# Kernel tuning notes

Hardware: AMD Instinct MI355X
Metric: run time of the kernel (lower is better)

The kernel has to match this reference:

```python
import jax, jax.numpy as jnp
import numpy as np

N_NODES = 100000
N_EDGES = 1600000
F_IN = 64
CONVS = [128, 128, 64]
DECODER_HID = 128
N_CLASSES = 2


def _glorot(key, shape):
    fan_in = shape[1]
    lim = 1.0 / np.sqrt(fan_in)
    return jax.random.uniform(key, shape, jnp.float32, -lim, lim)


def setup_inputs() -> dict:
    key = jax.random.key(0)
    ks = jax.random.split(key, 16)
    x = jax.random.normal(ks[0], (N_NODES, F_IN), jnp.float32)
    edge_index = jax.random.randint(ks[1], (2, N_EDGES), 0, N_NODES, jnp.int32)
    dims = [F_IN] + CONVS  # [64,128,128,64]
    inp = {"x": x, "edge_index": edge_index}
    ki = 2
    for i in range(len(CONVS)):
        d_in, d_out = dims[i], dims[i + 1]
        inp[f"Wl{i}"] = _glorot(ks[ki], (d_out, d_in)); ki += 1
        inp[f"bl{i}"] = jnp.zeros((d_out,), jnp.float32)
        inp[f"Wr{i}"] = _glorot(ks[ki], (d_out, d_in)); ki += 1
    inp["Wd1"] = _glorot(ks[ki], (DECODER_HID, CONVS[-1])); ki += 1
    inp["bd1"] = jnp.zeros((DECODER_HID,), jnp.float32)
    inp["Wd2"] = _glorot(ks[ki], (N_CLASSES, DECODER_HID)); ki += 1
    inp["bd2"] = jnp.zeros((N_CLASSES,), jnp.float32)
    return inp


def _sage_conv(x, src, dst, inv_deg, Wl, bl, Wr):
    # gather source features per edge, scatter-mean onto destinations
    msg = x[src]                                          # [E, F]
    agg = jax.ops.segment_sum(msg, dst, num_segments=N_NODES)
    agg = agg * inv_deg[:, None]                          # mean aggregation
    # out = lin_l(mean_neighbors) + lin_r(x_self)
    return agg @ Wl.T + bl + x @ Wr.T


def reference(x, edge_index, Wl0, bl0, Wr0, Wl1, bl1, Wr1, Wl2, bl2, Wr2, Wd1, bd1, Wd2, bd2):
    src = edge_index[0]
    dst = edge_index[1]
    deg = jax.ops.segment_sum(jnp.ones((src.shape[0],), x.dtype), dst, num_segments=N_NODES)
    inv_deg = jnp.where(deg > 0, 1.0 / jnp.maximum(deg, 1.0), 0.0)
    params = [(Wl0, bl0, Wr0), (Wl1, bl1, Wr1), (Wl2, bl2, Wr2)]
    h = x
    for i, (Wl, bl, Wr) in enumerate(params):
        h = _sage_conv(h, src, dst, inv_deg, Wl, bl, Wr)
        if i != len(params) - 1:
            h = jax.nn.relu(h)
    # decoder: ReLU -> Linear(64,128) -> ReLU -> Linear(128,2)
    h = jax.nn.relu(h)
    h = jax.nn.relu(h @ Wd1.T + bd1)
    return h @ Wd2.T + bd2
```

## Files before the change

### kernel.cpp

```cpp
#include <hip/hip_runtime.h>
#include <cstdint>
#include <cstddef>

#define NN 100000
#define NE 1600000
#define BSH 9
#define NBUCK 196
#define P3_CHUNK 8192
#define P3_BLOCKS 196

typedef __attribute__((ext_vector_type(8))) short short8;
typedef __attribute__((ext_vector_type(4))) float f32x4;


__device__ inline unsigned pack_split(float v) {
    unsigned u = __builtin_bit_cast(unsigned, v);
    unsigned hi = (u + 0x7fffu + ((u >> 16) & 1u)) >> 16;
    float vh = __builtin_bit_cast(float, hi << 16);
    float r = v - vh;
    unsigned u2 = __builtin_bit_cast(unsigned, r);
    unsigned lo = (u2 + 0x7fffu + ((u2 >> 16) & 1u)) >> 16;
    return hi | (lo << 16);
}

__device__ inline float rec_sum(unsigned u) {
    return __builtin_bit_cast(float, u << 16) + __builtin_bit_cast(float, u & 0xffff0000u);
}

__device__ inline void frag_extract(const unsigned* p, short8& hi, short8& lo) {
    uint4 p0 = *(const uint4*)p;
    uint4 p1 = *(const uint4*)(p + 4);
    unsigned h0 = __builtin_amdgcn_perm(p0.y, p0.x, 0x05040100u);
    unsigned l0 = __builtin_amdgcn_perm(p0.y, p0.x, 0x07060302u);
    unsigned h1 = __builtin_amdgcn_perm(p0.w, p0.z, 0x05040100u);
    unsigned l1 = __builtin_amdgcn_perm(p0.w, p0.z, 0x07060302u);
    unsigned h2 = __builtin_amdgcn_perm(p1.y, p1.x, 0x05040100u);
    unsigned l2 = __builtin_amdgcn_perm(p1.y, p1.x, 0x07060302u);
    unsigned h3 = __builtin_amdgcn_perm(p1.w, p1.z, 0x05040100u);
    unsigned l3 = __builtin_amdgcn_perm(p1.w, p1.z, 0x07060302u);
    uint4 H = {h0, h1, h2, h3};
    uint4 L = {l0, l1, l2, l3};
    hi = __builtin_bit_cast(short8, H);
    lo = __builtin_bit_cast(short8, L);
}


__global__ __launch_bounds__(256) void k_zero_small(int* p, int n) {
    for (int i = threadIdx.x; i < n; i += 256) p[i] = 0;
}

__global__ __launch_bounds__(256) void k_hist(const int* __restrict__ dst, int* __restrict__ bcnt) {
    __shared__ int h[NBUCK];
    const int tid = threadIdx.x;
    if (tid < NBUCK) h[tid] = 0;
    __syncthreads();
    for (int e = blockIdx.x * 256 + tid; e < NE; e += gridDim.x * 256)
        atomicAdd(&h[dst[e] >> BSH], 1);
    __syncthreads();
    if (tid < NBUCK) atomicAdd(&bcnt[tid], h[tid]);
}

__global__ __launch_bounds__(256) void k_bscan(const int* __restrict__ bcnt, int* __restrict__ bstart,
                                               int* __restrict__ gcur) {
    __shared__ int sh[256];
    const int t = threadIdx.x;
    int v = (t < NBUCK) ? bcnt[t] : 0;
    sh[t] = v;
    __syncthreads();
    for (int off = 1; off < 256; off <<= 1) {
        int u = 0;
        if (t >= off) u = sh[t - off];
        __syncthreads();
        sh[t] += u;
        __syncthreads();
    }
    int excl = sh[t] - v;
    if (t < NBUCK) { bstart[t] = excl; gcur[t] = excl; }
    if (t == 0) bstart[NBUCK] = NE;
}

__global__ __launch_bounds__(256) void k_partition(const int* __restrict__ srce, const int* __restrict__ dste,
                                                   int* __restrict__ gcur, int* __restrict__ tmp) {
    __shared__ int h[NBUCK], lstart[NBUCK], gbase[NBUCK], scn[256];
    __shared__ int s_pack[P3_CHUNK];
    __shared__ int s_gad[P3_CHUNK];
    const int tid = threadIdx.x;
    const int base = blockIdx.x * P3_CHUNK;
    if (tid < NBUCK) h[tid] = 0;
    __syncthreads();
    int rank[P3_CHUNK / 256];
#pragma unroll
    for (int i = 0; i < P3_CHUNK / 256; i++) {
        int idx = base + i * 256 + tid;
        if (idx < NE) rank[i] = atomicAdd(&h[dste[idx] >> BSH], 1);
    }
    __syncthreads();
    int hv = (tid < NBUCK) ? h[tid] : 0;
    if (tid < NBUCK) gbase[tid] = atomicAdd(&gcur[tid], hv);
    scn[tid] = hv;
    __syncthreads();
    for (int off = 1; off < 256; off <<= 1) {
        int u = 0;
        if (tid >= off) u = scn[tid - off];
        __syncthreads();
        scn[tid] += u;
        __syncthreads();
    }
    if (tid < NBUCK) lstart[tid] = scn[tid] - hv;
    __syncthreads();
#pragma unroll
    for (int i = 0; i < P3_CHUNK / 256; i++) {
        int idx = base + i * 256 + tid;
        if (idx < NE) {
            int d = dste[idx], s = srce[idx];
            int b = d >> BSH;
            int slot = lstart[b] + rank[i];
            s_pack[slot] = (s << BSH) | (d & ((1 << BSH) - 1));
            s_gad[slot] = gbase[b] + rank[i];
        }
    }
    __syncthreads();
    int chunkN = NE - base;
    if (chunkN > P3_CHUNK) chunkN = P3_CHUNK;
#pragma unroll
    for (int i = 0; i < P3_CHUNK / 256; i++) {
        int slot = i * 256 + tid;
        if (slot < chunkN) tmp[s_gad[slot]] = s_pack[slot];
    }
}

__global__ __launch_bounds__(256) void k_bucket(const int* __restrict__ tmp, const int* __restrict__ bstart,
                                                int* __restrict__ row_ptr, int* __restrict__ col,
                                                float* __restrict__ invd) {
    __shared__ int cnt[512], cur[512], scn[256];
    const int b = blockIdx.x, tid = threadIdx.x;
    const int base = bstart[b];
    const int n = bstart[b + 1] - base;
    cnt[tid] = 0;
    cnt[tid + 256] = 0;
    __syncthreads();
    for (int k = tid; k < n; k += 256) atomicAdd(&cnt[tmp[base + k] & 511], 1);
    __syncthreads();
    int c0 = cnt[2 * tid], c1 = cnt[2 * tid + 1], s = c0 + c1;
    scn[tid] = s;
    __syncthreads();
    for (int off = 1; off < 256; off <<= 1) {
        int u = 0;
        if (tid >= off) u = scn[tid - off];
        __syncthreads();
        scn[tid] += u;
        __syncthreads();
    }
    int excl = scn[tid] - s;
    int node = (b << BSH) + 2 * tid;
    if (node < NN) {
        row_ptr[node] = base + excl;
        invd[node] = c0 ? 1.0f / (float)c0 : 0.0f;
    }
    if (node + 1 < NN) {
        row_ptr[node + 1] = base + excl + c0;
        invd[node + 1] = c1 ? 1.0f / (float)c1 : 0.0f;
    }
    cur[2 * tid] = base + excl;
    cur[2 * tid + 1] = base + excl + c0;
    if (b == 0 && tid == 0) row_ptr[NN] = NE;
    __syncthreads();
    for (int k = tid; k < n; k += 256) {
        int p = tmp[base + k];
        int pos = atomicAdd(&cur[p & 511], 1);
        col[pos] = p >> BSH;
    }
}


__global__ __launch_bounds__(256) void k_xsplit(const float* __restrict__ x, unsigned* __restrict__ Xp) {
    int i = blockIdx.x * 256 + threadIdx.x;
    float4 v = ((const float4*)x)[i];
    uint4 o = {pack_split(v.x), pack_split(v.y), pack_split(v.z), pack_split(v.w)};
    ((uint4*)Xp)[i] = o;
}

__global__ __launch_bounds__(256) void k_wsplit(const float* __restrict__ Wl0, const float* __restrict__ Wr0,
                                                const float* __restrict__ Wl1, const float* __restrict__ Wr1,
                                                const float* __restrict__ Wl2, const float* __restrict__ Wr2,
                                                const float* __restrict__ Wd1, const float* __restrict__ bl2,
                                                unsigned* __restrict__ Wp, float* __restrict__ biasPQ) {
    int i = blockIdx.x * 256 + threadIdx.x;
    if (i < 8192) Wp[i] = pack_split(Wl0[i]);
    else if (i < 16384) Wp[i] = pack_split(Wr0[i - 8192]);
    else if (i < 32768) Wp[i] = pack_split(Wl1[i - 16384]);
    else if (i < 49152) Wp[i] = pack_split(Wr1[i - 32768]);
    else if (i < 57344) Wp[i] = pack_split(Wl2[i - 49152]);
    else if (i < 65536) Wp[i] = pack_split(Wr2[i - 57344]);
    else if (i < 73728) Wp[i] = pack_split(Wd1[i - 65536]);
    else if (i < 73856) {
        int j = i - 73728;
        biasPQ[j] = (j < 64) ? 0.f : bl2[j - 64];
    }
}


__global__ __launch_bounds__(256) void k_agg64(const float* __restrict__ h, const int* __restrict__ row_ptr,
                                               const int* __restrict__ col, const float* __restrict__ inv_deg,
                                               unsigned* __restrict__ agg) {
    int node = blockIdx.x * 4 + (threadIdx.x >> 6);
    int lane = threadIdx.x & 63;
    int start = row_ptr[node], end = row_ptr[node + 1];
    float a0 = 0.f, a1 = 0.f, a2 = 0.f, a3 = 0.f, a4 = 0.f, a5 = 0.f, a6 = 0.f, a7 = 0.f;
    for (int cs = start; cs < end; cs += 64) {
        int n = end - cs;
        if (n > 64) n = 64;
        int my = (lane < n) ? col[cs + lane] : 0;
        int j = 0;
        for (; j + 8 <= n; j += 8) {
            int s0 = __shfl(my, j + 0), s1 = __shfl(my, j + 1);
            int s2 = __shfl(my, j + 2), s3 = __shfl(my, j + 3);
            int s4 = __shfl(my, j + 4), s5 = __shfl(my, j + 5);
            int s6 = __shfl(my, j + 6), s7 = __shfl(my, j + 7);
            float v0 = h[(size_t)s0 * 64 + lane];
            float v1 = h[(size_t)s1 * 64 + lane];
            float v2 = h[(size_t)s2 * 64 + lane];
            float v3 = h[(size_t)s3 * 64 + lane];
            float v4 = h[(size_t)s4 * 64 + lane];
            float v5 = h[(size_t)s5 * 64 + lane];
            float v6 = h[(size_t)s6 * 64 + lane];
            float v7 = h[(size_t)s7 * 64 + lane];
            a0 += v0; a1 += v1; a2 += v2; a3 += v3;
            a4 += v4; a5 += v5; a6 += v6; a7 += v7;
        }
        for (; j < n; j++) {
            int s = __shfl(my, j);
            a0 += h[(size_t)s * 64 + lane];
        }
    }
    float acc = ((a0 + a1) + (a2 + a3)) + ((a4 + a5) + (a6 + a7));
    agg[(size_t)node * 64 + lane] = pack_split(acc * inv_deg[node]);
}

__global__ __launch_bounds__(256) void k_agg128p(const unsigned* __restrict__ hp, const int* __restrict__ row_ptr,
                                                 const int* __restrict__ col, const float* __restrict__ inv_deg,
                                                 unsigned* __restrict__ agg) {
    int node = blockIdx.x * 4 + (threadIdx.x >> 6);
    int lane = threadIdx.x & 63;
    int start = row_ptr[node], end = row_ptr[node + 1];
    const uint2* h2 = (const uint2*)hp;
    float ax0 = 0.f, ax1 = 0.f, ax2 = 0.f, ax3 = 0.f, ax4 = 0.f, ax5 = 0.f, ax6 = 0.f, ax7 = 0.f;
    float ay0 = 0.f, ay1 = 0.f, ay2 = 0.f, ay3 = 0.f, ay4 = 0.f, ay5 = 0.f, ay6 = 0.f, ay7 = 0.f;
    for (int cs = start; cs < end; cs += 64) {
        int n = end - cs;
        if (n > 64) n = 64;
        int my = (lane < n) ? col[cs + lane] : 0;
        int j = 0;
        for (; j + 8 <= n; j += 8) {
            int s0 = __shfl(my, j + 0), s1 = __shfl(my, j + 1);
            int s2 = __shfl(my, j + 2), s3 = __shfl(my, j + 3);
            int s4 = __shfl(my, j + 4), s5 = __shfl(my, j + 5);
            int s6 = __shfl(my, j + 6), s7 = __shfl(my, j + 7);
            uint2 u0 = h2[(size_t)s0 * 64 + lane];
            uint2 u1 = h2[(size_t)s1 * 64 + lane];
            uint2 u2 = h2[(size_t)s2 * 64 + lane];
            uint2 u3 = h2[(size_t)s3 * 64 + lane];
            uint2 u4 = h2[(size_t)s4 * 64 + lane];
            uint2 u5 = h2[(size_t)s5 * 64 + lane];
            uint2 u6 = h2[(size_t)s6 * 64 + lane];
            uint2 u7 = h2[(size_t)s7 * 64 + lane];
            ax0 += rec_sum(u0.x); ay0 += rec_sum(u0.y);
            ax1 += rec_sum(u1.x); ay1 += rec_sum(u1.y);
            ax2 += rec_sum(u2.x); ay2 += rec_sum(u2.y);
            ax3 += rec_sum(u3.x); ay3 += rec_sum(u3.y);
            ax4 += rec_sum(u4.x); ay4 += rec_sum(u4.y);
            ax5 += rec_sum(u5.x); ay5 += rec_sum(u5.y);
            ax6 += rec_sum(u6.x); ay6 += rec_sum(u6.y);
            ax7 += rec_sum(u7.x); ay7 += rec_sum(u7.y);
        }
        for (; j < n; j++) {
            int s = __shfl(my, j);
            uint2 u = h2[(size_t)s * 64 + lane];
            ax0 += rec_sum(u.x);
            ay0 += rec_sum(u.y);
        }
    }
    float w = inv_deg[node];
    float sx = (((ax0 + ax1) + (ax2 + ax3)) + ((ax4 + ax5) + (ax6 + ax7))) * w;
    float sy = (((ay0 + ay1) + (ay2 + ay3)) + ((ay4 + ay5) + (ay6 + ay7))) * w;
    uint2 o = {pack_split(sx), pack_split(sy)};
    *((uint2*)agg + (size_t)node * 64 + lane) = o;
}

__global__ __launch_bounds__(256) void k_agg_relu64p(const float* __restrict__ PQ, const int* __restrict__ row_ptr,
                                                     const int* __restrict__ col, const float* __restrict__ inv_deg,
                                                     unsigned* __restrict__ out) {
    int node = blockIdx.x * 4 + (threadIdx.x >> 6);
    int lane = threadIdx.x & 63;
    int start = row_ptr[node], end = row_ptr[node + 1];
    float a0 = 0.f, a1 = 0.f, a2 = 0.f, a3 = 0.f, a4 = 0.f, a5 = 0.f, a6 = 0.f, a7 = 0.f;
    for (int cs = start; cs < end; cs += 64) {
        int n = end - cs;
        if (n > 64) n = 64;
        int my = (lane < n) ? col[cs + lane] : 0;
        int j = 0;
        for (; j + 8 <= n; j += 8) {
            int s0 = __shfl(my, j + 0), s1 = __shfl(my, j + 1);
            int s2 = __shfl(my, j + 2), s3 = __shfl(my, j + 3);
            int s4 = __shfl(my, j + 4), s5 = __shfl(my, j + 5);
            int s6 = __shfl(my, j + 6), s7 = __shfl(my, j + 7);
            float v0 = PQ[(size_t)s0 * 128 + lane];
            float v1 = PQ[(size_t)s1 * 128 + lane];
            float v2 = PQ[(size_t)s2 * 128 + lane];
            float v3 = PQ[(size_t)s3 * 128 + lane];
            float v4 = PQ[(size_t)s4 * 128 + lane];
            float v5 = PQ[(size_t)s5 * 128 + lane];
            float v6 = PQ[(size_t)s6 * 128 + lane];
            float v7 = PQ[(size_t)s7 * 128 + lane];
            a0 += v0; a1 += v1; a2 += v2; a3 += v3;
            a4 += v4; a5 += v5; a6 += v6; a7 += v7;
        }
        for (; j < n; j++) {
            int s = __shfl(my, j);
            a0 += PQ[(size_t)s * 128 + lane];
        }
    }
    float acc = ((a0 + a1) + (a2 + a3)) + ((a4 + a5) + (a6 + a7));
    float v = PQ[(size_t)node * 128 + 64 + lane] + inv_deg[node] * acc;
    out[(size_t)node * 64 + lane] = pack_split(fmaxf(v, 0.f));
}


#define LDL 36

template <int K>
__device__ inline void mg_phase(const unsigned* __restrict__ A, const unsigned* __restrict__ W,
                                int m0, unsigned* Al, unsigned* Bl, f32x4 (&acc)[4][4],
                                int tid, int wm, int wn, int l15, int quad) {
    const int srow = tid >> 1, scol = (tid & 1) * 16;
#pragma unroll 1
    for (int kt = 0; kt < K; kt += 32) {
        __syncthreads();
        uint4 a0 = {0, 0, 0, 0}, a1 = {0, 0, 0, 0}, a2 = {0, 0, 0, 0}, a3 = {0, 0, 0, 0};
        int gr = m0 + srow;
        if (gr < NN) {
            const uint4* p = (const uint4*)(A + (size_t)gr * K + kt + scol);
            a0 = p[0]; a1 = p[1]; a2 = p[2]; a3 = p[3];
        }
        const uint4* q = (const uint4*)(W + srow * K + kt + scol);
        uint4 b0 = q[0], b1 = q[1], b2 = q[2], b3 = q[3];
        uint4* da = (uint4*)(Al + srow * LDL + scol);
        da[0] = a0; da[1] = a1; da[2] = a2; da[3] = a3;
        uint4* db = (uint4*)(Bl + srow * LDL + scol);
        db[0] = b0; db[1] = b1; db[2] = b2; db[3] = b3;
        __syncthreads();
        short8 ah[4], al[4], bh[4], bl[4];
#pragma unroll
        for (int t = 0; t < 4; t++) {
            frag_extract(Al + (wm + t * 16 + l15) * LDL + quad * 8, ah[t], al[t]);
            frag_extract(Bl + (wn + t * 16 + l15) * LDL + quad * 8, bh[t], bl[t]);
        }
#pragma unroll
        for (int mt = 0; mt < 4; mt++)
#pragma unroll
            for (int nt = 0; nt < 4; nt++) {
                acc[mt][nt] = __builtin_amdgcn_mfma_f32_16x16x32_bf16(ah[mt], bh[nt], acc[mt][nt], 0, 0, 0);
                acc[mt][nt] = __builtin_amdgcn_mfma_f32_16x16x32_bf16(ah[mt], bl[nt], acc[mt][nt], 0, 0, 0);
                acc[mt][nt] = __builtin_amdgcn_mfma_f32_16x16x32_bf16(al[mt], bh[nt], acc[mt][nt], 0, 0, 0);
            }
    }
}

template <int K1, int K2, bool RELU, int OMODE>
__global__ __launch_bounds__(256) void k_mgemm(const unsigned* __restrict__ A1, const unsigned* __restrict__ W1,
                                               const unsigned* A2, const unsigned* __restrict__ W2,
                                               const float* __restrict__ bias, float* Cf, unsigned* Cp) {
    __shared__ unsigned Al[128 * LDL];
    __shared__ unsigned Bl[128 * LDL];
    const int tid = threadIdx.x;
    const int m0 = blockIdx.x * 128;
    const int wave = tid >> 6, lane = tid & 63;
    const int wm = (wave & 1) * 64, wn = (wave >> 1) * 64;
    const int l15 = lane & 15, quad = lane >> 4;
    f32x4 acc[4][4];
#pragma unroll
    for (int i = 0; i < 4; i++)
#pragma unroll
        for (int j = 0; j < 4; j++) acc[i][j] = (f32x4){0.f, 0.f, 0.f, 0.f};

    mg_phase<K1>(A1, W1, m0, Al, Bl, acc, tid, wm, wn, l15, quad);
    if (K2 > 0) mg_phase<K2>(A2, W2, m0, Al, Bl, acc, tid, wm, wn, l15, quad);

#pragma unroll
    for (int mt = 0; mt < 4; mt++) {
        int rbase = m0 + wm + mt * 16 + quad * 4;
#pragma unroll
        for (int nt = 0; nt < 4; nt++) {
            int cg = wn + nt * 16 + l15;
            float bv = bias[cg];
#pragma unroll
            for (int r = 0; r < 4; r++) {
                int row = rbase + r;
                if (row < NN) {
                    float v = acc[mt][nt][r] + bv;
                    if (RELU) v = fmaxf(v, 0.f);
                    if (OMODE == 0) Cf[(size_t)row * 128 + cg] = v;
                    else Cp[(size_t)row * 128 + cg] = pack_split(v);
                }
            }
        }
    }
}


__global__ __launch_bounds__(256) void k_dec2(const float* __restrict__ h, const float* __restrict__ W,
                                              const float* __restrict__ b, float* __restrict__ out) {
    int node = blockIdx.x * 4 + (threadIdx.x >> 6);
    int lane = threadIdx.x & 63;
    float2 hv = *((const float2*)(h + (size_t)node * 128) + lane);
    float d0 = hv.x * W[2 * lane] + hv.y * W[2 * lane + 1];
    float d1 = hv.x * W[128 + 2 * lane] + hv.y * W[128 + 2 * lane + 1];
    for (int off = 32; off > 0; off >>= 1) {
        d0 += __shfl_down(d0, off);
        d1 += __shfl_down(d1, off);
    }
    if (lane == 0) {
        out[(size_t)node * 2 + 0] = d0 + b[0];
        out[(size_t)node * 2 + 1] = d1 + b[1];
    }
}


extern "C" void kernel_launch(void* const* d_in, const int* in_sizes, int n_in,
                              void* d_out, int out_size, void* d_ws, size_t ws_size,
                              hipStream_t stream) {
    const float* x   = (const float*)d_in[0];
    const int*   ei  = (const int*)d_in[1];
    const float* Wl0 = (const float*)d_in[2];
    const float* bl0 = (const float*)d_in[3];
    const float* Wr0 = (const float*)d_in[4];
    const float* Wl1 = (const float*)d_in[5];
    const float* bl1 = (const float*)d_in[6];
    const float* Wr1 = (const float*)d_in[7];
    const float* Wl2 = (const float*)d_in[8];
    const float* bl2 = (const float*)d_in[9];
    const float* Wr2 = (const float*)d_in[10];
    const float* Wd1 = (const float*)d_in[11];
    const float* bd1 = (const float*)d_in[12];
    const float* Wd2 = (const float*)d_in[13];
    const float* bd2 = (const float*)d_in[14];
    float* out = (float*)d_out;

    char* ws = (char*)d_ws;
    size_t off = 0;
    auto alloc = [&](size_t bytes) {
        char* p = ws + off;
        off = (off + bytes + 255) & ~(size_t)255;
        return p;
    };
    int*      bcnt    = (int*)alloc((size_t)NBUCK * 4);
    int*      bstart  = (int*)alloc((size_t)(NBUCK + 1) * 4);
    int*      gcur    = (int*)alloc((size_t)NBUCK * 4);
    int*      row_ptr = (int*)alloc((size_t)(NN + 1) * 4);
    float*    invd    = (float*)alloc((size_t)NN * 4);
    int*      col     = (int*)alloc((size_t)NE * 4);
    unsigned* Wp      = (unsigned*)alloc((size_t)73728 * 4);
    float*    biasPQ  = (float*)alloc(128 * 4);
    unsigned* S1      = (unsigned*)alloc((size_t)NN * 128 * 4);
    unsigned* S2      = (unsigned*)alloc((size_t)NN * 128 * 4);
    (void)ws_size;

    int*      tmp   = (int*)S2;
    unsigned* Xp    = S1;
    unsigned* Agg0p = S1 + (size_t)NN * 64;
    unsigned* G0p   = S2;
    unsigned* Agg1p = S1;
    unsigned* H1p   = S2;
    float*    PQ    = (float*)S1;
    unsigned* h2p   = S2;
    float*    d1    = (float*)S1;

    const unsigned* WL0p = Wp;
    const unsigned* WR0p = Wp + 8192;
    const unsigned* WL1p = Wp + 16384;
    const unsigned* WR1p = Wp + 32768;
    const unsigned* WPQp = Wp + 49152;
    const unsigned* WD1p = Wp + 65536;

    const int* srce = ei;
    const int* dste = ei + NE;

    k_zero_small<<<1, 256, 0, stream>>>(bcnt, NBUCK);
    k_hist<<<400, 256, 0, stream>>>(dste, bcnt);
    k_bscan<<<1, 256, 0, stream>>>(bcnt, bstart, gcur);
    k_partition<<<P3_BLOCKS, 256, 0, stream>>>(srce, dste, gcur, tmp);
    k_bucket<<<NBUCK, 256, 0, stream>>>(tmp, bstart, row_ptr, col, invd);

    k_wsplit<<<289, 256, 0, stream>>>(Wl0, Wr0, Wl1, Wr1, Wl2, Wr2, Wd1, bl2, Wp, biasPQ);
    k_xsplit<<<(NN * 64 / 4 + 255) / 256, 256, 0, stream>>>(x, Xp);

    const int gGemm = (NN + 127) / 128;
    const int gNode = NN / 4;

    k_agg64<<<gNode, 256, 0, stream>>>(x, row_ptr, col, invd, Agg0p);
    k_mgemm<64, 64, true, 1><<<gGemm, 256, 0, stream>>>(Agg0p, WL0p, Xp, WR0p, bl0, nullptr, G0p);

    k_agg128p<<<gNode, 256, 0, stream>>>(G0p, row_ptr, col, invd, Agg1p);
    k_mgemm<128, 128, true, 1><<<gGemm, 256, 0, stream>>>(Agg1p, WL1p, G0p, WR1p, bl1, nullptr, H1p);

    k_mgemm<128, 0, false, 0><<<gGemm, 256, 0, stream>>>(H1p, WPQp, nullptr, nullptr, biasPQ, PQ, nullptr);
    k_agg_relu64p<<<gNode, 256, 0, stream>>>(PQ, row_ptr, col, invd, h2p);

    k_mgemm<64, 0, true, 0><<<gGemm, 256, 0, stream>>>(h2p, WD1p, nullptr, nullptr, bd1, d1, nullptr);
    k_dec2<<<gNode, 256, 0, stream>>>(d1, Wd2, bd2, out);
}
```

Before: 548.3 us.

## Gather bf16-high features in aggregations and store hi/lo planes separately

```diff
diff --git a/kernel.cpp b/kernel.cpp
--- a/kernel.cpp
+++ b/kernel.cpp
@@ -23,25 +23,13 @@
     return hi | (lo << 16);
 }
 
-__device__ inline float rec_sum(unsigned u) {
-    return __builtin_bit_cast(float, u << 16) + __builtin_bit_cast(float, u & 0xffff0000u);
-}
-
-__device__ inline void frag_extract(const unsigned* p, short8& hi, short8& lo) {
-    uint4 p0 = *(const uint4*)p;
-    uint4 p1 = *(const uint4*)(p + 4);
-    unsigned h0 = __builtin_amdgcn_perm(p0.y, p0.x, 0x05040100u);
-    unsigned l0 = __builtin_amdgcn_perm(p0.y, p0.x, 0x07060302u);
-    unsigned h1 = __builtin_amdgcn_perm(p0.w, p0.z, 0x05040100u);
-    unsigned l1 = __builtin_amdgcn_perm(p0.w, p0.z, 0x07060302u);
-    unsigned h2 = __builtin_amdgcn_perm(p1.y, p1.x, 0x05040100u);
-    unsigned l2 = __builtin_amdgcn_perm(p1.y, p1.x, 0x07060302u);
-    unsigned h3 = __builtin_amdgcn_perm(p1.w, p1.z, 0x05040100u);
-    unsigned l3 = __builtin_amdgcn_perm(p1.w, p1.z, 0x07060302u);
-    uint4 H = {h0, h1, h2, h3};
-    uint4 L = {l0, l1, l2, l3};
-    hi = __builtin_bit_cast(short8, H);
-    lo = __builtin_bit_cast(short8, L);
+__device__ inline unsigned short rnb(float v) {
+    unsigned u = __builtin_bit_cast(unsigned, v);
+    return (unsigned short)((u + 0x7fffu + ((u >> 16) & 1u)) >> 16);
+}
+
+__device__ inline float bf2f(unsigned short u) {
+    return __builtin_bit_cast(float, (unsigned)u << 16);
 }
 
 
@@ -173,36 +161,45 @@
 }
 
 
-__global__ __launch_bounds__(256) void k_xsplit(const float* __restrict__ x, unsigned* __restrict__ Xp) {
+__global__ __launch_bounds__(256) void k_xhi(const float* __restrict__ x, unsigned short* __restrict__ Xh) {
     int i = blockIdx.x * 256 + threadIdx.x;
     float4 v = ((const float4*)x)[i];
-    uint4 o = {pack_split(v.x), pack_split(v.y), pack_split(v.z), pack_split(v.w)};
-    ((uint4*)Xp)[i] = o;
+    ushort4 o = {rnb(v.x), rnb(v.y), rnb(v.z), rnb(v.w)};
+    ((ushort4*)Xh)[i] = o;
 }
 
 __global__ __launch_bounds__(256) void k_wsplit(const float* __restrict__ Wl0, const float* __restrict__ Wr0,
                                                 const float* __restrict__ Wl1, const float* __restrict__ Wr1,
                                                 const float* __restrict__ Wl2, const float* __restrict__ Wr2,
                                                 const float* __restrict__ Wd1, const float* __restrict__ bl2,
-                                                unsigned* __restrict__ Wp, float* __restrict__ biasPQ) {
+                                                unsigned short* __restrict__ Wh, unsigned short* __restrict__ Wl,
+                                                float* __restrict__ biasPQ) {
     int i = blockIdx.x * 256 + threadIdx.x;
-    if (i < 8192) Wp[i] = pack_split(Wl0[i]);
-    else if (i < 16384) Wp[i] = pack_split(Wr0[i - 8192]);
-    else if (i < 32768) Wp[i] = pack_split(Wl1[i - 16384]);
-    else if (i < 49152) Wp[i] = pack_split(Wr1[i - 32768]);
-    else if (i < 57344) Wp[i] = pack_split(Wl2[i - 49152]);
-    else if (i < 65536) Wp[i] = pack_split(Wr2[i - 57344]);
-    else if (i < 73728) Wp[i] = pack_split(Wd1[i - 65536]);
-    else if (i < 73856) {
+    float v = 0.f;
+    bool valid = true;
+    if (i < 8192) v = Wl0[i];
+    else if (i < 16384) v = Wr0[i - 8192];
+    else if (i < 32768) v = Wl1[i - 16384];
+    else if (i < 49152) v = Wr1[i - 32768];
+    else if (i < 57344) v = Wl2[i - 49152];
+    else if (i < 65536) v = Wr2[i - 57344];
+    else if (i < 73728) v = Wd1[i - 65536];
+    else valid = false;
+    if (valid) {
+        unsigned ps = pack_split(v);
+        Wh[i] = (unsigned short)ps;
+        Wl[i] = (unsigned short)(ps >> 16);
+    }
+    if (i >= 73728 && i < 73856) {
         int j = i - 73728;
         biasPQ[j] = (j < 64) ? 0.f : bl2[j - 64];
     }
 }
 
 
-__global__ __launch_bounds__(256) void k_agg64(const float* __restrict__ h, const int* __restrict__ row_ptr,
-                                               const int* __restrict__ col, const float* __restrict__ inv_deg,
-                                               unsigned* __restrict__ agg) {
+__global__ __launch_bounds__(256) void k_agg64h(const unsigned short* __restrict__ Xh, const int* __restrict__ row_ptr,
+                                                const int* __restrict__ col, const float* __restrict__ invd,
+                                                unsigned short* __restrict__ Ah, unsigned short* __restrict__ Al) {
     int node = blockIdx.x * 4 + (threadIdx.x >> 6);
     int lane = threadIdx.x & 63;
     int start = row_ptr[node], end = row_ptr[node + 1];
@@ -217,33 +214,34 @@
             int s2 = __shfl(my, j + 2), s3 = __shfl(my, j + 3);
             int s4 = __shfl(my, j + 4), s5 = __shfl(my, j + 5);
             int s6 = __shfl(my, j + 6), s7 = __shfl(my, j + 7);
-            float v0 = h[(size_t)s0 * 64 + lane];
-            float v1 = h[(size_t)s1 * 64 + lane];
-            float v2 = h[(size_t)s2 * 64 + lane];
-            float v3 = h[(size_t)s3 * 64 + lane];
-            float v4 = h[(size_t)s4 * 64 + lane];
-            float v5 = h[(size_t)s5 * 64 + lane];
-            float v6 = h[(size_t)s6 * 64 + lane];
-            float v7 = h[(size_t)s7 * 64 + lane];
+            float v0 = bf2f(Xh[(size_t)s0 * 64 + lane]);
+            float v1 = bf2f(Xh[(size_t)s1 * 64 + lane]);
+            float v2 = bf2f(Xh[(size_t)s2 * 64 + lane]);
+            float v3 = bf2f(Xh[(size_t)s3 * 64 + lane]);
+            float v4 = bf2f(Xh[(size_t)s4 * 64 + lane]);
+            float v5 = bf2f(Xh[(size_t)s5 * 64 + lane]);
+            float v6 = bf2f(Xh[(size_t)s6 * 64 + lane]);
+            float v7 = bf2f(Xh[(size_t)s7 * 64 + lane]);
             a0 += v0; a1 += v1; a2 += v2; a3 += v3;
             a4 += v4; a5 += v5; a6 += v6; a7 += v7;
         }
         for (; j < n; j++) {
             int s = __shfl(my, j);
-            a0 += h[(size_t)s * 64 + lane];
+            a0 += bf2f(Xh[(size_t)s * 64 + lane]);
         }
     }
     float acc = ((a0 + a1) + (a2 + a3)) + ((a4 + a5) + (a6 + a7));
-    agg[(size_t)node * 64 + lane] = pack_split(acc * inv_deg[node]);
-}
-
-__global__ __launch_bounds__(256) void k_agg128p(const unsigned* __restrict__ hp, const int* __restrict__ row_ptr,
-                                                 const int* __restrict__ col, const float* __restrict__ inv_deg,
-                                                 unsigned* __restrict__ agg) {
+    unsigned ps = pack_split(acc * invd[node]);
+    Ah[(size_t)node * 64 + lane] = (unsigned short)ps;
+    Al[(size_t)node * 64 + lane] = (unsigned short)(ps >> 16);
+}
+
+__global__ __launch_bounds__(256) void k_agg128h(const unsigned short* __restrict__ Gh, const int* __restrict__ row_ptr,
+                                                 const int* __restrict__ col, const float* __restrict__ invd,
+                                                 unsigned short* __restrict__ Ah, unsigned short* __restrict__ Al) {
     int node = blockIdx.x * 4 + (threadIdx.x >> 6);
     int lane = threadIdx.x & 63;
     int start = row_ptr[node], end = row_ptr[node + 1];
-    const uint2* h2 = (const uint2*)hp;
     float ax0 = 0.f, ax1 = 0.f, ax2 = 0.f, ax3 = 0.f, ax4 = 0.f, ax5 = 0.f, ax6 = 0.f, ax7 = 0.f;
     float ay0 = 0.f, ay1 = 0.f, ay2 = 0.f, ay3 = 0.f, ay4 = 0.f, ay5 = 0.f, ay6 = 0.f, ay7 = 0.f;
     for (int cs = start; cs < end; cs += 64) {
@@ -256,40 +254,42 @@
             int s2 = __shfl(my, j + 2), s3 = __shfl(my, j + 3);
             int s4 = __shfl(my, j + 4), s5 = __shfl(my, j + 5);
             int s6 = __shfl(my, j + 6), s7 = __shfl(my, j + 7);
-            uint2 u0 = h2[(size_t)s0 * 64 + lane];
-            uint2 u1 = h2[(size_t)s1 * 64 + lane];
-            uint2 u2 = h2[(size_t)s2 * 64 + lane];
-            uint2 u3 = h2[(size_t)s3 * 64 + lane];
-            uint2 u4 = h2[(size_t)s4 * 64 + lane];
-            uint2 u5 = h2[(size_t)s5 * 64 + lane];
-            uint2 u6 = h2[(size_t)s6 * 64 + lane];
-            uint2 u7 = h2[(size_t)s7 * 64 + lane];
-            ax0 += rec_sum(u0.x); ay0 += rec_sum(u0.y);
-            ax1 += rec_sum(u1.x); ay1 += rec_sum(u1.y);
-            ax2 += rec_sum(u2.x); ay2 += rec_sum(u2.y);
-            ax3 += rec_sum(u3.x); ay3 += rec_sum(u3.y);
-            ax4 += rec_sum(u4.x); ay4 += rec_sum(u4.y);
-            ax5 += rec_sum(u5.x); ay5 += rec_sum(u5.y);
-            ax6 += rec_sum(u6.x); ay6 += rec_sum(u6.y);
-            ax7 += rec_sum(u7.x); ay7 += rec_sum(u7.y);
+            unsigned u0 = *(const unsigned*)(Gh + (size_t)s0 * 128 + 2 * lane);
+            unsigned u1 = *(const unsigned*)(Gh + (size_t)s1 * 128 + 2 * lane);
+            unsigned u2 = *(const unsigned*)(Gh + (size_t)s2 * 128 + 2 * lane);
+            unsigned u3 = *(const unsigned*)(Gh + (size_t)s3 * 128 + 2 * lane);
+            unsigned u4 = *(const unsigned*)(Gh + (size_t)s4 * 128 + 2 * lane);
+            unsigned u5 = *(const unsigned*)(Gh + (size_t)s5 * 128 + 2 * lane);
+            unsigned u6 = *(const unsigned*)(Gh + (size_t)s6 * 128 + 2 * lane);
+            unsigned u7 = *(const unsigned*)(Gh + (size_t)s7 * 128 + 2 * lane);
+            ax0 += bf2f((unsigned short)u0); ay0 += bf2f((unsigned short)(u0 >> 16));
+            ax1 += bf2f((unsigned short)u1); ay1 += bf2f((unsigned short)(u1 >> 16));
+            ax2 += bf2f((unsigned short)u2); ay2 += bf2f((unsigned short)(u2 >> 16));
+            ax3 += bf2f((unsigned short)u3); ay3 += bf2f((unsigned short)(u3 >> 16));
+            ax4 += bf2f((unsigned short)u4); ay4 += bf2f((unsigned short)(u4 >> 16));
+            ax5 += bf2f((unsigned short)u5); ay5 += bf2f((unsigned short)(u5 >> 16));
+            ax6 += bf2f((unsigned short)u6); ay6 += bf2f((unsigned short)(u6 >> 16));
+            ax7 += bf2f((unsigned short)u7); ay7 += bf2f((unsigned short)(u7 >> 16));
         }
         for (; j < n; j++) {
             int s = __shfl(my, j);
-            uint2 u = h2[(size_t)s * 64 + lane];
-            ax0 += rec_sum(u.x);
-            ay0 += rec_sum(u.y);
-        }
-    }
-    float w = inv_deg[node];
+            unsigned u = *(const unsigned*)(Gh + (size_t)s * 128 + 2 * lane);
+            ax0 += bf2f((unsigned short)u);
+            ay0 += bf2f((unsigned short)(u >> 16));
+        }
+    }
+    float w = invd[node];
     float sx = (((ax0 + ax1) + (ax2 + ax3)) + ((ax4 + ax5) + (ax6 + ax7))) * w;
     float sy = (((ay0 + ay1) + (ay2 + ay3)) + ((ay4 + ay5) + (ay6 + ay7))) * w;
-    uint2 o = {pack_split(sx), pack_split(sy)};
-    *((uint2*)agg + (size_t)node * 64 + lane) = o;
-}
-
-__global__ __launch_bounds__(256) void k_agg_relu64p(const float* __restrict__ PQ, const int* __restrict__ row_ptr,
-                                                     const int* __restrict__ col, const float* __restrict__ inv_deg,
-                                                     unsigned* __restrict__ out) {
+    unsigned px = pack_split(sx), py = pack_split(sy);
+    *(unsigned*)(Ah + (size_t)node * 128 + 2 * lane) = (px & 0xffffu) | (py << 16);
+    *(unsigned*)(Al + (size_t)node * 128 + 2 * lane) = (px >> 16) | (py & 0xffff0000u);
+}
+
+__global__ __launch_bounds__(256) void k_aggPh(const unsigned short* __restrict__ Ph, const float* __restrict__ Qf,
+                                               const int* __restrict__ row_ptr, const int* __restrict__ col,
+                                               const float* __restrict__ invd,
+                                               unsigned short* __restrict__ Hh, unsigned short* __restrict__ Hl) {
     int node = blockIdx.x * 4 + (threadIdx.x >> 6);
     int lane = threadIdx.x & 63;
     int start = row_ptr[node], end = row_ptr[node + 1];
@@ -304,56 +304,85 @@
             int s2 = __shfl(my, j + 2), s3 = __shfl(my, j + 3);
             int s4 = __shfl(my, j + 4), s5 = __shfl(my, j + 5);
             int s6 = __shfl(my, j + 6), s7 = __shfl(my, j + 7);
-            float v0 = PQ[(size_t)s0 * 128 + lane];
-            float v1 = PQ[(size_t)s1 * 128 + lane];
-            float v2 = PQ[(size_t)s2 * 128 + lane];
-            float v3 = PQ[(size_t)s3 * 128 + lane];
-            float v4 = PQ[(size_t)s4 * 128 + lane];
-            float v5 = PQ[(size_t)s5 * 128 + lane];
-            float v6 = PQ[(size_t)s6 * 128 + lane];
-            float v7 = PQ[(size_t)s7 * 128 + lane];
+            float v0 = bf2f(Ph[(size_t)s0 * 64 + lane]);
+            float v1 = bf2f(Ph[(size_t)s1 * 64 + lane]);
+            float v2 = bf2f(Ph[(size_t)s2 * 64 + lane]);
+            float v3 = bf2f(Ph[(size_t)s3 * 64 + lane]);
+            float v4 = bf2f(Ph[(size_t)s4 * 64 + lane]);
+            float v5 = bf2f(Ph[(size_t)s5 * 64 + lane]);
+            float v6 = bf2f(Ph[(size_t)s6 * 64 + lane]);
+            float v7 = bf2f(Ph[(size_t)s7 * 64 + lane]);
             a0 += v0; a1 += v1; a2 += v2; a3 += v3;
             a4 += v4; a5 += v5; a6 += v6; a7 += v7;
         }
         for (; j < n; j++) {
             int s = __shfl(my, j);
-            a0 += PQ[(size_t)s * 128 + lane];
+            a0 += bf2f(Ph[(size_t)s * 64 + lane]);
         }
     }
     float acc = ((a0 + a1) + (a2 + a3)) + ((a4 + a5) + (a6 + a7));
-    float v = PQ[(size_t)node * 128 + 64 + lane] + inv_deg[node] * acc;
-    out[(size_t)node * 64 + lane] = pack_split(fmaxf(v, 0.f));
-}
-
-
-#define LDL 36
-
-template <int K>
-__device__ inline void mg_phase(const unsigned* __restrict__ A, const unsigned* __restrict__ W,
-                                int m0, unsigned* Al, unsigned* Bl, f32x4 (&acc)[4][4],
-                                int tid, int wm, int wn, int l15, int quad) {
-    const int srow = tid >> 1, scol = (tid & 1) * 16;
+    float v = Qf[(size_t)node * 64 + lane] + invd[node] * acc;
+    unsigned ps = pack_split(fmaxf(v, 0.f));
+    Hh[(size_t)node * 64 + lane] = (unsigned short)ps;
+    Hl[(size_t)node * 64 + lane] = (unsigned short)(ps >> 16);
+}
+
+
+#define LA 40
+
+template <int K, int AFMT>
+__device__ inline void mgp(const unsigned short* __restrict__ Ah_g, const unsigned short* __restrict__ Al_g,
+                           const float* __restrict__ Af_g,
+                           const unsigned short* __restrict__ Wh_g, const unsigned short* __restrict__ Wl_g,
+                           int m0, unsigned short* sAh, unsigned short* sAl,
+                           unsigned short* sBh, unsigned short* sBl,
+                           f32x4 (&acc)[4][4], int tid, int wm, int wn, int l15, int quad) {
+    const int srow = tid >> 1, sc = (tid & 1) * 16;
 #pragma unroll 1
     for (int kt = 0; kt < K; kt += 32) {
         __syncthreads();
-        uint4 a0 = {0, 0, 0, 0}, a1 = {0, 0, 0, 0}, a2 = {0, 0, 0, 0}, a3 = {0, 0, 0, 0};
         int gr = m0 + srow;
-        if (gr < NN) {
-            const uint4* p = (const uint4*)(A + (size_t)gr * K + kt + scol);
-            a0 = p[0]; a1 = p[1]; a2 = p[2]; a3 = p[3];
-        }
-        const uint4* q = (const uint4*)(W + srow * K + kt + scol);
-        uint4 b0 = q[0], b1 = q[1], b2 = q[2], b3 = q[3];
-        uint4* da = (uint4*)(Al + srow * LDL + scol);
-        da[0] = a0; da[1] = a1; da[2] = a2; da[3] = a3;
-        uint4* db = (uint4*)(Bl + srow * LDL + scol);
-        db[0] = b0; db[1] = b1; db[2] = b2; db[3] = b3;
+        uint4 h0 = {0, 0, 0, 0}, h1 = {0, 0, 0, 0}, l0 = {0, 0, 0, 0}, l1 = {0, 0, 0, 0};
+        if (AFMT == 0) {
+            if (gr < NN) {
+                const uint4* ph = (const uint4*)(Ah_g + (size_t)gr * K + kt + sc);
+                h0 = ph[0]; h1 = ph[1];
+                const uint4* pl = (const uint4*)(Al_g + (size_t)gr * K + kt + sc);
+                l0 = pl[0]; l1 = pl[1];
+            }
+        } else {
+            if (gr < NN) {
+                const float4* pf = (const float4*)(Af_g + (size_t)gr * K + kt + sc);
+                float4 f0 = pf[0], f1 = pf[1], f2 = pf[2], f3 = pf[3];
+                float fs[16] = {f0.x, f0.y, f0.z, f0.w, f1.x, f1.y, f1.z, f1.w,
+                                f2.x, f2.y, f2.z, f2.w, f3.x, f3.y, f3.z, f3.w};
+                alignas(16) unsigned short hh[16], ll[16];
+#pragma unroll
+                for (int i = 0; i < 16; i++) {
+                    unsigned ps = pack_split(fs[i]);
+                    hh[i] = (unsigned short)ps;
+                    ll[i] = (unsigned short)(ps >> 16);
+                }
+                h0 = *(const uint4*)&hh[0]; h1 = *(const uint4*)&hh[8];
+                l0 = *(const uint4*)&ll[0]; l1 = *(const uint4*)&ll[8];
+            }
+        }
+        const uint4* qh = (const uint4*)(Wh_g + srow * K + kt + sc);
+        uint4 b0 = qh[0], b1 = qh[1];
+        const uint4* ql = (const uint4*)(Wl_g + srow * K + kt + sc);
+        uint4 b2 = ql[0], b3 = ql[1];
+        *(uint4*)(sAh + srow * LA + sc) = h0; *(uint4*)(sAh + srow * LA + sc + 8) = h1;
+        *(uint4*)(sAl + srow * LA + sc) = l0; *(uint4*)(sAl + srow * LA + sc + 8) = l1;
+        *(uint4*)(sBh + srow * LA + sc) = b0; *(uint4*)(sBh + srow * LA + sc + 8) = b1;
+        *(uint4*)(sBl + srow * LA + sc) = b2; *(uint4*)(sBl + srow * LA + sc + 8) = b3;
         __syncthreads();
         short8 ah[4], al[4], bh[4], bl[4];
 #pragma unroll
         for (int t = 0; t < 4; t++) {
-            frag_extract(Al + (wm + t * 16 + l15) * LDL + quad * 8, ah[t], al[t]);
-            frag_extract(Bl + (wn + t * 16 + l15) * LDL + quad * 8, bh[t], bl[t]);
+            ah[t] = *(const short8*)(sAh + (wm + t * 16 + l15) * LA + quad * 8);
+            al[t] = *(const short8*)(sAl + (wm + t * 16 + l15) * LA + quad * 8);
+            bh[t] = *(const short8*)(sBh + (wn + t * 16 + l15) * LA + quad * 8);
+            bl[t] = *(const short8*)(sBl + (wn + t * 16 + l15) * LA + quad * 8);
         }
 #pragma unroll
         for (int mt = 0; mt < 4; mt++)
@@ -366,12 +395,15 @@
     }
 }
 
-template <int K1, int K2, bool RELU, int OMODE>
-__global__ __launch_bounds__(256) void k_mgemm(const unsigned* __restrict__ A1, const unsigned* __restrict__ W1,
-                                               const unsigned* A2, const unsigned* __restrict__ W2,
-                                               const float* __restrict__ bias, float* Cf, unsigned* Cp) {
-    __shared__ unsigned Al[128 * LDL];
-    __shared__ unsigned Bl[128 * LDL];
+template <int K1, int K2, int AF1, int AF2, bool RELU, int OMODE>
+__global__ __launch_bounds__(256) void k_mgemm(
+    const unsigned short* A1h, const unsigned short* A1l, const float* A1f,
+    const unsigned short* A2h, const unsigned short* A2l, const float* A2f,
+    const unsigned short* __restrict__ W1h, const unsigned short* __restrict__ W1l,
+    const unsigned short* __restrict__ W2h, const unsigned short* __restrict__ W2l,
+    const float* __restrict__ bias, float* Cf, unsigned short* Chi, unsigned short* Clo,
+    unsigned short* Ph, float* Qf) {
+    __shared__ unsigned short sAh[128 * LA], sAl[128 * LA], sBh[128 * LA], sBl[128 * LA];
     const int tid = threadIdx.x;
     const int m0 = blockIdx.x * 128;
     const int wave = tid >> 6, lane = tid & 63;
@@ -383,8 +415,8 @@
 #pragma unroll
         for (int j = 0; j < 4; j++) acc[i][j] = (f32x4){0.f, 0.f, 0.f, 0.f};
 
-    mg_phase<K1>(A1, W1, m0, Al, Bl, acc, tid, wm, wn, l15, quad);
-    if (K2 > 0) mg_phase<K2>(A2, W2, m0, Al, Bl, acc, tid, wm, wn, l15, quad);
+    mgp<K1, AF1>(A1h, A1l, A1f, W1h, W1l, m0, sAh, sAl, sBh, sBl, acc, tid, wm, wn, l15, quad);
+    if (K2 > 0) mgp<K2, AF2>(A2h, A2l, A2f, W2h, W2l, m0, sAh, sAl, sBh, sBl, acc, tid, wm, wn, l15, quad);
 
 #pragma unroll
     for (int mt = 0; mt < 4; mt++) {
@@ -399,8 +431,16 @@
                 if (row < NN) {
                     float v = acc[mt][nt][r] + bv;
                     if (RELU) v = fmaxf(v, 0.f);
-                    if (OMODE == 0) Cf[(size_t)row * 128 + cg] = v;
-                    else Cp[(size_t)row * 128 + cg] = pack_split(v);
+                    if (OMODE == 0) {
+                        Cf[(size_t)row * 128 + cg] = v;
+                    } else if (OMODE == 1) {
+                        unsigned ps = pack_split(v);
+                        Chi[(size_t)row * 128 + cg] = (unsigned short)ps;
+                        Clo[(size_t)row * 128 + cg] = (unsigned short)(ps >> 16);
+                    } else {
+                        if (cg < 64) Ph[(size_t)row * 64 + cg] = rnb(v);
+                        else Qf[(size_t)row * 64 + cg - 64] = v;
+                    }
                 }
             }
         }
@@ -453,34 +493,41 @@
         off = (off + bytes + 255) & ~(size_t)255;
         return p;
     };
-    int*      bcnt    = (int*)alloc((size_t)NBUCK * 4);
-    int*      bstart  = (int*)alloc((size_t)(NBUCK + 1) * 4);
-    int*      gcur    = (int*)alloc((size_t)NBUCK * 4);
-    int*      row_ptr = (int*)alloc((size_t)(NN + 1) * 4);
-    float*    invd    = (float*)alloc((size_t)NN * 4);
-    int*      col     = (int*)alloc((size_t)NE * 4);
-    unsigned* Wp      = (unsigned*)alloc((size_t)73728 * 4);
-    float*    biasPQ  = (float*)alloc(128 * 4);
-    unsigned* S1      = (unsigned*)alloc((size_t)NN * 128 * 4);
-    unsigned* S2      = (unsigned*)alloc((size_t)NN * 128 * 4);
+    int*            bcnt    = (int*)alloc((size_t)NBUCK * 4);
+    int*            bstart  = (int*)alloc((size_t)(NBUCK + 1) * 4);
+    int*            gcur    = (int*)alloc((size_t)NBUCK * 4);
+    int*            row_ptr = (int*)alloc((size_t)(NN + 1) * 4);
+    float*          invd    = (float*)alloc((size_t)NN * 4);
+    float*          biasPQ  = (float*)alloc(128 * 4);
+    unsigned short* Wh      = (unsigned short*)alloc((size_t)73728 * 2);
+    unsigned short* Wl      = (unsigned short*)alloc((size_t)73728 * 2);
+    int*            col     = (int*)alloc((size_t)NE * 4);
+    char*           R1      = alloc((size_t)NN * 128 * 4);
+    char*           R2      = alloc((size_t)NN * 128 * 4);
     (void)ws_size;
 
-    int*      tmp   = (int*)S2;
-    unsigned* Xp    = S1;
-    unsigned* Agg0p = S1 + (size_t)NN * 64;
-    unsigned* G0p   = S2;
-    unsigned* Agg1p = S1;
-    unsigned* H1p   = S2;
-    float*    PQ    = (float*)S1;
-    unsigned* h2p   = S2;
-    float*    d1    = (float*)S1;
-
-    const unsigned* WL0p = Wp;
-    const unsigned* WR0p = Wp + 8192;
-    const unsigned* WL1p = Wp + 16384;
-    const unsigned* WR1p = Wp + 32768;
-    const unsigned* WPQp = Wp + 49152;
-    const unsigned* WD1p = Wp + 65536;
+    int*            tmp   = (int*)R1;
+    unsigned short* Xh    = (unsigned short*)R1;
+    unsigned short* Agg0h = (unsigned short*)(R1 + 12800000);
+    unsigned short* Agg0l = (unsigned short*)(R1 + 25600000);
+    unsigned short* Agg1h = (unsigned short*)R1;
+    unsigned short* Agg1l = (unsigned short*)(R1 + 25600000);
+    unsigned short* Ph    = (unsigned short*)R1;
+    float*          Qf    = (float*)(R1 + 12800000);
+    float*          d1    = (float*)R1;
+    unsigned short* G0h   = (unsigned short*)R2;
+    unsigned short* G0l   = (unsigned short*)(R2 + 25600000);
+    unsigned short* H1h   = G0h;
+    unsigned short* H1l   = G0l;
+    unsigned short* h2h   = (unsigned short*)R2;
+    unsigned short* h2l   = (unsigned short*)(R2 + 12800000);
+
+    const unsigned short* WL0h = Wh,         * WL0l = Wl;
+    const unsigned short* WR0h = Wh + 8192,  * WR0l = Wl + 8192;
+    const unsigned short* WL1h = Wh + 16384, * WL1l = Wl + 16384;
+    const unsigned short* WR1h = Wh + 32768, * WR1l = Wl + 32768;
+    const unsigned short* WPQh = Wh + 49152, * WPQl = Wl + 49152;
+    const unsigned short* WD1h = Wh + 65536, * WD1l = Wl + 65536;
 
     const int* srce = ei;
     const int* dste = ei + NE;
@@ -491,21 +538,29 @@
     k_partition<<<P3_BLOCKS, 256, 0, stream>>>(srce, dste, gcur, tmp);
     k_bucket<<<NBUCK, 256, 0, stream>>>(tmp, bstart, row_ptr, col, invd);
 
-    k_wsplit<<<289, 256, 0, stream>>>(Wl0, Wr0, Wl1, Wr1, Wl2, Wr2, Wd1, bl2, Wp, biasPQ);
-    k_xsplit<<<(NN * 64 / 4 + 255) / 256, 256, 0, stream>>>(x, Xp);
+    k_wsplit<<<289, 256, 0, stream>>>(Wl0, Wr0, Wl1, Wr1, Wl2, Wr2, Wd1, bl2, Wh, Wl, biasPQ);
+    k_xhi<<<(NN * 64 / 4 + 255) / 256, 256, 0, stream>>>(x, Xh);
 
     const int gGemm = (NN + 127) / 128;
     const int gNode = NN / 4;
 
-    k_agg64<<<gNode, 256, 0, stream>>>(x, row_ptr, col, invd, Agg0p);
-    k_mgemm<64, 64, true, 1><<<gGemm, 256, 0, stream>>>(Agg0p, WL0p, Xp, WR0p, bl0, nullptr, G0p);
-
-    k_agg128p<<<gNode, 256, 0, stream>>>(G0p, row_ptr, col, invd, Agg1p);
-    k_mgemm<128, 128, true, 1><<<gGemm, 256, 0, stream>>>(Agg1p, WL1p, G0p, WR1p, bl1, nullptr, H1p);
-
-    k_mgemm<128, 0, false, 0><<<gGemm, 256, 0, stream>>>(H1p, WPQp, nullptr, nullptr, biasPQ, PQ, nullptr);
-    k_agg_relu64p<<<gNode, 256, 0, stream>>>(PQ, row_ptr, col, invd, h2p);
-
-    k_mgemm<64, 0, true, 0><<<gGemm, 256, 0, stream>>>(h2p, WD1p, nullptr, nullptr, bd1, d1, nullptr);
+    k_agg64h<<<gNode, 256, 0, stream>>>(Xh, row_ptr, col, invd, Agg0h, Agg0l);
+    k_mgemm<64, 64, 0, 1, true, 1><<<gGemm, 256, 0, stream>>>(
+        Agg0h, Agg0l, nullptr, nullptr, nullptr, x,
+        WL0h, WL0l, WR0h, WR0l, bl0, nullptr, G0h, G0l, nullptr, nullptr);
+
+    k_agg128h<<<gNode, 256, 0, stream>>>(G0h, row_ptr, col, invd, Agg1h, Agg1l);
+    k_mgemm<128, 128, 0, 0, true, 1><<<gGemm, 256, 0, stream>>>(
+        Agg1h, Agg1l, nullptr, G0h, G0l, nullptr,
+        WL1h, WL1l, WR1h, WR1l, bl1, nullptr, H1h, H1l, nullptr, nullptr);
+
+    k_mgemm<128, 0, 0, 0, false, 2><<<gGemm, 256, 0, stream>>>(
+        H1h, H1l, nullptr, nullptr, nullptr, nullptr,
+        WPQh, WPQl, nullptr, nullptr, biasPQ, nullptr, nullptr, nullptr, Ph, Qf);
+    k_aggPh<<<gNode, 256, 0, stream>>>(Ph, Qf, row_ptr, col, invd, h2h, h2l);
+
+    k_mgemm<64, 0, 0, 0, true, 0><<<gGemm, 256, 0, stream>>>(
+        h2h, h2l, nullptr, nullptr, nullptr, nullptr,
+        WD1h, WD1l, nullptr, nullptr, bd1, d1, nullptr, nullptr, nullptr, nullptr);
     k_dec2<<<gNode, 256, 0, stream>>>(d1, Wd2, bd2, out);
 }
```

Result: faster. 488.5 us (-10.9%).
